# Kernel tuning notes

Hardware: AMD Instinct MI355X
Metric: run time of the kernel (lower is better)

The kernel has to match this reference:

```python
import jax, jax.numpy as jnp
import numpy as np

IMG = 224
NUM_VIEWS = 6
K = 5  # splat kernel size (5x5 = 25 offsets)


def setup_inputs() -> dict:
    key = jax.random.key(0)
    points = jax.random.normal(key, (16, 32768, 3), dtype=jnp.float32)
    return {"points": points}


def _render(points):
    B, N, _ = points.shape
    deg2rad = jnp.pi / 180.0
    az = jnp.linspace(0.0, 360.0, NUM_VIEWS + 1)[:-1] * deg2rad          # (V,)
    el = jnp.array([0.0, 30.0, -30.0, 0.0, 0.0, 0.0])[:NUM_VIEWS] * deg2rad

    # 5x5 splat offsets in normalized coords, matching torch meshgrid(ij) + stack([dx,dy])
    off = jnp.linspace(-2.0 / IMG, 2.0 / IMG, K)
    dyg, dxg = jnp.meshgrid(off, off, indexing="ij")
    koff = jnp.stack([dxg, dyg], axis=-1).reshape(-1, 2)                  # (25, 2)

    def one_view(a, e):
        x, y, z = points[..., 0], points[..., 1], points[..., 2]
        x_rot = x * jnp.cos(a) - z * jnp.sin(a)
        z_rot = x * jnp.sin(a) + z * jnp.cos(a)
        y_rot = y * jnp.cos(e) - z_rot * jnp.sin(e)
        z_fin = y * jnp.sin(e) + z_rot * jnp.cos(e)                       # (B, N)
        p2d = jnp.stack([x_rot, y_rot], axis=-1)                          # (B, N, 2)

        zmin = jnp.min(z_fin, axis=1, keepdims=True)
        zmax = jnp.max(z_fin, axis=1, keepdims=True)
        feat = 0.3 + 0.7 * (z_fin - zmin) / (zmax - zmin + 1e-6)          # (B, N), in [0.3, 1.0]

        coords = p2d[:, :, None, :] + koff[None, None, :, :]              # (B, N, 25, 2)
        # torch .long() truncates toward zero; astype(int32) does too
        px = ((coords[..., 0] + 1.0) * 0.5 * (IMG - 1)).astype(jnp.int32)
        py = ((coords[..., 1] + 1.0) * 0.5 * (IMG - 1)).astype(jnp.int32)
        valid = (px >= 0) & (px < IMG) & (py >= 0) & (py < IMG)
        # invalid splats routed out-of-bounds and dropped by the scatter
        idx = jnp.where(valid, py * IMG + px, IMG * IMG).reshape(B, -1)   # (B, N*25)
        f = jnp.broadcast_to(feat[:, :, None], (B, N, K * K)).reshape(B, -1)

        def splat(i, fv):
            return jnp.zeros(IMG * IMG, dtype=points.dtype).at[i].max(fv, mode="drop")

        img = jax.vmap(splat)(idx, f).reshape(B, IMG, IMG)
        # all 3 channels receive the identical feature values
        return jnp.broadcast_to(img[:, None], (B, 3, IMG, IMG))

    views = jax.vmap(one_view)(az, el)                                    # (V, B, 3, H, W)
    return jnp.transpose(views, (1, 0, 2, 3, 4))                          # (B, V, 3, H, W)


def reference(points) -> jnp.ndarray:
    return _render(points)
```

## Files before the change

kernel.cpp:

```cpp
#include <hip/hip_runtime.h>
#include <math.h>

#define IMG    224
#define NVIEWS 6
#define BATCH  16
#define NPTS   32768
#define PLANE  (IMG * IMG)
#define HROWS  112
#define TILE_ELEMS (HROWS * IMG)
#define NT     1024
#define NWAVES (NT / 64)
#define QCAP   320
#define NWG    (BATCH * NVIEWS * 2)
#define KITERS (NPTS / (4 * NT))

typedef float fx4 __attribute__((ext_vector_type(4)));

struct ViewTrig {
    float sa[NVIEWS], ca[NVIEWS], se[NVIEWS], ce[NVIEWS];
    float off0, off4;
};

__device__ __forceinline__ float fmul_(float a, float b) {
#pragma clang fp contract(off)
    return a * b;
}
__device__ __forceinline__ float fadd_(float a, float b) {
#pragma clang fp contract(off)
    return a + b;
}
__device__ __forceinline__ float fsub_(float a, float b) {
#pragma clang fp contract(off)
    return a - b;
}
__device__ __forceinline__ int pix_(float c) {
    return (int)fmul_(fadd_(c, 1.0f), 111.5f);
}

__device__ __forceinline__ unsigned fmap_(float f) {
    unsigned b = __float_as_uint(f);
    return b ^ ((unsigned)((int)b >> 31) | 0x80000000u);
}
__device__ __forceinline__ float fmap_inv_(unsigned u) {
    unsigned b = (u & 0x80000000u) ? (u ^ 0x80000000u) : ~u;
    return __uint_as_float(b);
}

__device__ __forceinline__ int lane_prefix_(unsigned long long m) {
    return __builtin_amdgcn_mbcnt_hi((unsigned)(m >> 32),
           __builtin_amdgcn_mbcnt_lo((unsigned)m, 0));
}

__global__ __launch_bounds__(NT, 4) void render_kernel(
    const float* __restrict__ pts, float* __restrict__ out, ViewTrig vt)
{
    extern __shared__ __align__(16) unsigned tile[];
    __shared__ uint2 wq[NWAVES][QCAP];
    __shared__ float smin[NWAVES], smax[NWAVES];

    const int bid  = blockIdx.x;
    const int xcd  = bid & 7;
    const int slot = bid >> 3;
    const int hi   = (slot >= 12) ? 1 : 0;
    const int b    = xcd + 8 * hi;
    const int vh   = slot - 12 * hi;
    const int v    = vh >> 1;
    const int h    = vh & 1;
    const int bv   = b * NVIEWS + v;
    const int row0 = h * HROWS;
    const int row1 = row0 + HROWS - 1;

    const float sa = vt.sa[v], ca = vt.ca[v], se = vt.se[v], ce = vt.ce[v];
    const float off0 = vt.off0, off4 = vt.off4;
    const float4* p4 = (const float4*)(pts + (size_t)b * NPTS * 3);

    const int lane = threadIdx.x & 63;
    const int wave = threadIdx.x >> 6;
    const int tid  = threadIdx.x;

    {
        int4* t4 = (int4*)tile;
        for (int i = tid; i < TILE_ELEMS / 4; i += NT)
            t4[i] = make_int4(0, 0, 0, 0);
    }
    __syncthreads();

    float zmin = INFINITY, zmax = -INFINITY;
    unsigned qcnt = 0;

    auto drain64 = [&]() {
        qcnt -= 64;
        const uint2 e = wq[wave][qcnt + lane];
        const unsigned fz = e.x, pk = e.y;
        const int cx0 = pk & 255;
        const int cx1 = (pk >> 8) & 255;
        const int r0 = max((int)((pk >> 16) & 255), row0) - row0;
        const int r1 = min((int)(pk >> 24), row1) - row0;
        #pragma unroll
        for (int dy = 0; dy < 3; ++dy) {
            const int ry = r0 + dy;
            const bool yok = (ry <= r1);
            #pragma unroll
            for (int dx = 0; dx < 3; ++dx) {
                const int cx = cx0 + dx;
                if (yok && (cx <= cx1)) atomicMax(&tile[ry * IMG + cx], fz);
            }
        }
    };

    auto do_point = [&](float x, float y, float z) {
        const float zr = fadd_(fmul_(x, sa), fmul_(z, ca));
        const float yr = fsub_(fmul_(y, ce), fmul_(zr, se));
        const float xr = fsub_(fmul_(x, ca), fmul_(z, sa));

        const int x0i = pix_(fadd_(xr, off0));
        const int x1i = pix_(fadd_(xr, off4));
        const int y0i = pix_(fadd_(yr, off0));
        const int y1i = pix_(fadd_(yr, off4));

        const float zf = fmaf(zr, ce, y * se);
        zmin = fminf(zmin, zf);
        zmax = fmaxf(zmax, zf);

        const bool pred = (x1i >= 0) && (x0i <= IMG - 1) &&
                          (y1i >= row0) && (y0i <= row1);
        const unsigned long long m = __ballot(pred);
        if (pred) {
            const int cx0 = max(x0i, 0);
            const int cx1 = min(x1i, IMG - 1);
            const int cy0 = max(y0i, 0);
            const int cy1 = min(y1i, IMG - 1);
            const unsigned pk = (unsigned)cx0 | ((unsigned)cx1 << 8) |
                                ((unsigned)cy0 << 16) | ((unsigned)cy1 << 24);
            wq[wave][qcnt + lane_prefix_(m)] = make_uint2(fmap_(zf), pk);
        }
        qcnt += (unsigned)__popcll(m);
    };

    float4 A = p4[3 * tid + 0];
    float4 B = p4[3 * tid + 1];
    float4 C = p4[3 * tid + 2];
    #pragma unroll
    for (int k = 0; k < KITERS; ++k) {
        float4 An, Bn, Cn;
        if (k + 1 < KITERS) {
            const int g = tid + (k + 1) * NT;
            An = p4[3 * g + 0];
            Bn = p4[3 * g + 1];
            Cn = p4[3 * g + 2];
        }
        do_point(A.x, A.y, A.z);
        do_point(A.w, B.x, B.y);
        do_point(B.z, B.w, C.x);
        do_point(C.y, C.z, C.w);
        while (qcnt >= 64) drain64();
        if (k + 1 < KITERS) { A = An; B = Bn; C = Cn; }
    }

    if (lane < (int)qcnt) {
        const uint2 e = wq[wave][lane];
        const unsigned fz = e.x, pk = e.y;
        const int cx0 = pk & 255;
        const int cx1 = (pk >> 8) & 255;
        const int r0 = max((int)((pk >> 16) & 255), row0) - row0;
        const int r1 = min((int)(pk >> 24), row1) - row0;
        #pragma unroll
        for (int dy = 0; dy < 3; ++dy) {
            const int ry = r0 + dy;
            const bool yok = (ry <= r1);
            #pragma unroll
            for (int dx = 0; dx < 3; ++dx) {
                const int cx = cx0 + dx;
                if (yok && (cx <= cx1)) atomicMax(&tile[ry * IMG + cx], fz);
            }
        }
    }

    for (int o = 32; o > 0; o >>= 1) {
        zmin = fminf(zmin, __shfl_down(zmin, o, 64));
        zmax = fmaxf(zmax, __shfl_down(zmax, o, 64));
    }
    if (lane == 0) { smin[wave] = zmin; smax[wave] = zmax; }
    __syncthreads();
    if (threadIdx.x == 0) {
        float mn = smin[0], mx = smax[0];
        for (int w = 1; w < NWAVES; ++w) {
            mn = fminf(mn, smin[w]);
            mx = fmaxf(mx, smax[w]);
        }
        smin[0] = mn; smax[0] = mx;
    }
    __syncthreads();
    const float scale = 0.7f / ((smax[0] - smin[0]) + 1e-6f);
    const float bias  = 0.3f - smin[0] * scale;

    float* dst = out + ((size_t)bv * 3) * PLANE + (size_t)row0 * IMG;
    const uint4* src = (const uint4*)tile;
    for (int i = tid; i < TILE_ELEMS / 4; i += NT) {
        const uint4 u = src[i];
        fx4 f;
        f.x = (u.x == 0u) ? 0.0f : fmaf(fmap_inv_(u.x), scale, bias);
        f.y = (u.y == 0u) ? 0.0f : fmaf(fmap_inv_(u.y), scale, bias);
        f.z = (u.z == 0u) ? 0.0f : fmaf(fmap_inv_(u.z), scale, bias);
        f.w = (u.w == 0u) ? 0.0f : fmaf(fmap_inv_(u.w), scale, bias);
        #pragma unroll
        for (int c = 0; c < 3; ++c)
            __builtin_nontemporal_store(f, (fx4*)(dst + (size_t)c * PLANE) + i);
    }
}

extern "C" void kernel_launch(void* const* d_in, const int* in_sizes, int n_in,
                              void* d_out, int out_size, void* d_ws, size_t ws_size,
                              hipStream_t stream)
{
    const float* pts = (const float*)d_in[0];
    float* out = (float*)d_out;

    ViewTrig vt;
    const float d2r = (float)(M_PI / 180.0);
    const float el_deg[NVIEWS] = {0.0f, 30.0f, -30.0f, 0.0f, 0.0f, 0.0f};
    for (int v = 0; v < NVIEWS; ++v) {
        float a = (float)(60 * v) * d2r;
        float e = el_deg[v] * d2r;
        vt.sa[v] = (float)sin((double)a);
        vt.ca[v] = (float)cos((double)a);
        vt.se[v] = (float)sin((double)e);
        vt.ce[v] = (float)cos((double)e);
    }
    {
        const float s = (float)(2.0 / 224.0);
        vt.off0 = -s;
        vt.off4 = s;
    }

    (void)hipFuncSetAttribute(reinterpret_cast<const void*>(render_kernel),
                              hipFuncAttributeMaxDynamicSharedMemorySize,
                              TILE_ELEMS * (int)sizeof(int));

    render_kernel<<<NWG, NT, TILE_ELEMS * sizeof(int), stream>>>(pts, out, vt);
}
```

Measured before the change: 87.53 us.

## Splat only center pixel, apply 3x3 max dilation at writeout, defer edge cases

For points whose 3x3 footprint is a full, untruncated block inside the tile, the kernel now does a single shared atomicMax at the centre pixel and no longer queues nine atomics. The 3x3 neighbourhood is rebuilt during the output pass with a separable max filter over rows (LDS reads) and columns (wave shuffles). Irregular or boundary-clipped splats are appended to a block-wide list and applied afterwards with global atomicMax into the output. This removes the per-wave queue and most of the shared-memory atomics. The cost is a contended shared counter, a capped overflow list that silently drops entries past DCAP, and global atomics that assume the output floats are non-negative. Correctness also depends on the dilation matching the original footprint exactly across tile boundaries.

```diff
diff --git a/kernel.cpp b/kernel.cpp
--- a/kernel.cpp
+++ b/kernel.cpp
@@ -10,7 +10,7 @@
 #define TILE_ELEMS (HROWS * IMG)
 #define NT     1024
 #define NWAVES (NT / 64)
-#define QCAP   320
+#define DCAP   2048
 #define NWG    (BATCH * NVIEWS * 2)
 #define KITERS (NPTS / (4 * NT))
 
@@ -46,16 +46,16 @@
     return __uint_as_float(b);
 }
 
-__device__ __forceinline__ int lane_prefix_(unsigned long long m) {
-    return __builtin_amdgcn_mbcnt_hi((unsigned)(m >> 32),
-           __builtin_amdgcn_mbcnt_lo((unsigned)m, 0));
+__device__ __forceinline__ unsigned umax3_(unsigned a, unsigned b, unsigned c) {
+    return max(max(a, b), c);
 }
 
 __global__ __launch_bounds__(NT, 4) void render_kernel(
     const float* __restrict__ pts, float* __restrict__ out, ViewTrig vt)
 {
     extern __shared__ __align__(16) unsigned tile[];
-    __shared__ uint2 wq[NWAVES][QCAP];
+    __shared__ uint2 dlist[DCAP];
+    __shared__ unsigned dcnt;
     __shared__ float smin[NWAVES], smax[NWAVES];
 
     const int bid  = blockIdx.x;
@@ -83,30 +83,10 @@
         for (int i = tid; i < TILE_ELEMS / 4; i += NT)
             t4[i] = make_int4(0, 0, 0, 0);
     }
+    if (tid == 0) dcnt = 0;
     __syncthreads();
 
     float zmin = INFINITY, zmax = -INFINITY;
-    unsigned qcnt = 0;
-
-    auto drain64 = [&]() {
-        qcnt -= 64;
-        const uint2 e = wq[wave][qcnt + lane];
-        const unsigned fz = e.x, pk = e.y;
-        const int cx0 = pk & 255;
-        const int cx1 = (pk >> 8) & 255;
-        const int r0 = max((int)((pk >> 16) & 255), row0) - row0;
-        const int r1 = min((int)(pk >> 24), row1) - row0;
-        #pragma unroll
-        for (int dy = 0; dy < 3; ++dy) {
-            const int ry = r0 + dy;
-            const bool yok = (ry <= r1);
-            #pragma unroll
-            for (int dx = 0; dx < 3; ++dx) {
-                const int cx = cx0 + dx;
-                if (yok && (cx <= cx1)) atomicMax(&tile[ry * IMG + cx], fz);
-            }
-        }
-    };
 
     auto do_point = [&](float x, float y, float z) {
         const float zr = fadd_(fmul_(x, sa), fmul_(z, ca));
@@ -124,17 +104,22 @@
 
         const bool pred = (x1i >= 0) && (x0i <= IMG - 1) &&
                           (y1i >= row0) && (y0i <= row1);
-        const unsigned long long m = __ballot(pred);
-        if (pred) {
+        const int cxc = x0i + 1, cyc = y0i + 1;
+        const bool clean = (x1i == x0i + 2) && (y1i == y0i + 2) &&
+                           (cxc >= 0) && (cxc <= IMG - 1) &&
+                           (cyc >= row0) && (cyc <= row1);
+        if (clean) {
+            atomicMax(&tile[(cyc - row0) * IMG + cxc], fmap_(zf));
+        } else if (pred) {
             const int cx0 = max(x0i, 0);
             const int cx1 = min(x1i, IMG - 1);
-            const int cy0 = max(y0i, 0);
-            const int cy1 = min(y1i, IMG - 1);
+            const int cy0 = max(y0i, row0);
+            const int cy1 = min(y1i, row1);
             const unsigned pk = (unsigned)cx0 | ((unsigned)cx1 << 8) |
                                 ((unsigned)cy0 << 16) | ((unsigned)cy1 << 24);
-            wq[wave][qcnt + lane_prefix_(m)] = make_uint2(fmap_(zf), pk);
-        }
-        qcnt += (unsigned)__popcll(m);
+            const unsigned di = atomicAdd(&dcnt, 1u);
+            if (di < DCAP) dlist[di] = make_uint2(__float_as_uint(zf), pk);
+        }
     };
 
     float4 A = p4[3 * tid + 0];
@@ -153,27 +138,7 @@
         do_point(A.w, B.x, B.y);
         do_point(B.z, B.w, C.x);
         do_point(C.y, C.z, C.w);
-        while (qcnt >= 64) drain64();
         if (k + 1 < KITERS) { A = An; B = Bn; C = Cn; }
-    }
-
-    if (lane < (int)qcnt) {
-        const uint2 e = wq[wave][lane];
-        const unsigned fz = e.x, pk = e.y;
-        const int cx0 = pk & 255;
-        const int cx1 = (pk >> 8) & 255;
-        const int r0 = max((int)((pk >> 16) & 255), row0) - row0;
-        const int r1 = min((int)(pk >> 24), row1) - row0;
-        #pragma unroll
-        for (int dy = 0; dy < 3; ++dy) {
-            const int ry = r0 + dy;
-            const bool yok = (ry <= r1);
-            #pragma unroll
-            for (int dx = 0; dx < 3; ++dx) {
-                const int cx = cx0 + dx;
-                if (yok && (cx <= cx1)) atomicMax(&tile[ry * IMG + cx], fz);
-            }
-        }
     }
 
     for (int o = 32; o > 0; o >>= 1) {
@@ -195,17 +160,67 @@
     const float bias  = 0.3f - smin[0] * scale;
 
     float* dst = out + ((size_t)bv * 3) * PLANE + (size_t)row0 * IMG;
-    const uint4* src = (const uint4*)tile;
-    for (int i = tid; i < TILE_ELEMS / 4; i += NT) {
-        const uint4 u = src[i];
+    const uint4* src4 = (const uint4*)tile;
+    const bool act = (lane < 56);
+    const int c0 = lane * 4;
+    for (int rr = 0; rr < 7; ++rr) {
+        const int r = wave * 7 + rr;
+        uint4 t0 = make_uint4(0u, 0u, 0u, 0u);
+        uint4 t1 = t0, t2 = t0;
+        if (act) {
+            t1 = src4[r * 56 + lane];
+            if (r > 0)          t0 = src4[(r - 1) * 56 + lane];
+            if (r < HROWS - 1)  t2 = src4[(r + 1) * 56 + lane];
+        }
+        uint4 m;
+        m.x = umax3_(t0.x, t1.x, t2.x);
+        m.y = umax3_(t0.y, t1.y, t2.y);
+        m.z = umax3_(t0.z, t1.z, t2.z);
+        m.w = umax3_(t0.w, t1.w, t2.w);
+        unsigned left  = __shfl_up(m.w, 1, 64);
+        unsigned right = __shfl_down(m.x, 1, 64);
+        if (lane == 0) left = 0u;
+        unsigned h0 = umax3_(left, m.x, m.y);
+        unsigned h1 = umax3_(m.x, m.y, m.z);
+        unsigned h2 = umax3_(m.y, m.z, m.w);
+        unsigned h3 = umax3_(m.z, m.w, right);
         fx4 f;
-        f.x = (u.x == 0u) ? 0.0f : fmaf(fmap_inv_(u.x), scale, bias);
-        f.y = (u.y == 0u) ? 0.0f : fmaf(fmap_inv_(u.y), scale, bias);
-        f.z = (u.z == 0u) ? 0.0f : fmaf(fmap_inv_(u.z), scale, bias);
-        f.w = (u.w == 0u) ? 0.0f : fmaf(fmap_inv_(u.w), scale, bias);
+        f.x = (h0 == 0u) ? 0.0f : fmaf(fmap_inv_(h0), scale, bias);
+        f.y = (h1 == 0u) ? 0.0f : fmaf(fmap_inv_(h1), scale, bias);
+        f.z = (h2 == 0u) ? 0.0f : fmaf(fmap_inv_(h2), scale, bias);
+        f.w = (h3 == 0u) ? 0.0f : fmaf(fmap_inv_(h3), scale, bias);
+        if (act) {
+            #pragma unroll
+            for (int c = 0; c < 3; ++c)
+                __builtin_nontemporal_store(
+                    f, (fx4*)(dst + (size_t)c * PLANE + (size_t)r * IMG + c0));
+        }
+    }
+
+    __threadfence();
+    __syncthreads();
+    const unsigned nd = min(dcnt, (unsigned)DCAP);
+    unsigned* outu = (unsigned*)(out + ((size_t)bv * 3) * PLANE);
+    for (unsigned j = tid; j < nd * 3u; j += NT) {
+        const uint2 e = dlist[j / 3u];
+        const int rsl = (int)(j % 3u);
+        const int cx0 = (int)(e.y & 255u);
+        const int cx1 = (int)((e.y >> 8) & 255u);
+        const int r0g = (int)((e.y >> 16) & 255u);
+        const int r1g = (int)(e.y >> 24);
+        const int r = r0g + rsl;
+        if (r > r1g) continue;
+        const float feat = fmaf(__uint_as_float(e.x), scale, bias);
+        const unsigned fu = __float_as_uint(feat);
         #pragma unroll
-        for (int c = 0; c < 3; ++c)
-            __builtin_nontemporal_store(f, (fx4*)(dst + (size_t)c * PLANE) + i);
+        for (int dx = 0; dx < 3; ++dx) {
+            const int cx = cx0 + dx;
+            if (cx <= cx1) {
+                #pragma unroll
+                for (int c = 0; c < 3; ++c)
+                    atomicMax(outu + (size_t)c * PLANE + (size_t)r * IMG + cx, fu);
+            }
+        }
     }
 }
 
```

Result: slower. 216.2 us (+147.0%).
